# Kernel tuning notes

Measured on AMD Instinct MI355X. Metric: run time of the kernel, lower is better.

## Reference

```python
import jax, jax.numpy as jnp
import numpy as np

N, E, D, C, L, G = 50000, 1600000, 128, 10, 4, 512
BN_EPS = 1e-5


def setup_inputs() -> dict:
    key = jax.random.key(0)
    ks = jax.random.split(key, 16)
    s = 0.05  # weight init scale
    inp = {
        "x": jax.random.normal(ks[0], (N, D), dtype=jnp.float32),
        "edge_index": jax.random.randint(ks[1], (2, E), 0, N, dtype=jnp.int32),
        "batch": jnp.sort(jax.random.randint(ks[2], (N,), 0, G, dtype=jnp.int32)),
        "num_graphs": G,
        # GINConv inner MLP params (layer 0 input dim == D since num_features == num_hidden)
        "conv_W1": jax.random.normal(ks[3], (L, D, D), dtype=jnp.float32) * s,
        "conv_b1": jnp.zeros((L, D), dtype=jnp.float32),
        "conv_bn_g": jnp.ones((L, D), dtype=jnp.float32),
        "conv_bn_b": jnp.zeros((L, D), dtype=jnp.float32),
        "conv_W2": jax.random.normal(ks[4], (L, D, D), dtype=jnp.float32) * s,
        "conv_b2": jnp.zeros((L, D), dtype=jnp.float32),
        # outer BatchNorm after each conv
        "bn_g": jnp.ones((L, D), dtype=jnp.float32),
        "bn_b": jnp.zeros((L, D), dtype=jnp.float32),
        # per-scale classifier heads (L+1 of them; fcs[0] input dim == num_features == D)
        "fc_W": jax.random.normal(ks[5], (L + 1, D, C), dtype=jnp.float32) * s,
        "fc_b": jnp.zeros((L + 1, C), dtype=jnp.float32),
    }
    return inp


def _bn(h, g, b):
    # BatchNorm1d in training mode: batch stats over nodes, biased variance
    m = h.mean(axis=0)
    v = jnp.mean((h - m) ** 2, axis=0)
    return (h - m) * jax.lax.rsqrt(v + BN_EPS) * g + b


def reference(x, edge_index, batch, num_graphs, conv_W1, conv_b1, conv_bn_g,
              conv_bn_b, conv_W2, conv_b2, bn_g, bn_b, fc_W, fc_b):
    n_nodes = x.shape[0]
    src, dst = edge_index[0], edge_index[1]
    outs = [x]
    h = x
    for i in range(L):
        # GINConv (eps=0, aggr='add'): mlp(x + scatter_add of neighbor features)
        agg = jax.ops.segment_sum(h[src], dst, num_segments=n_nodes)  # [N, D]
        z = h + agg
        z = z @ conv_W1[i] + conv_b1[i]
        z = jax.nn.relu(_bn(z, conv_bn_g[i], conv_bn_b[i]))
        z = z @ conv_W2[i] + conv_b2[i]
        h = jax.nn.relu(_bn(z, bn_g[i], bn_b[i]))
        outs.append(h)
    out = None
    for i, o in enumerate(outs):
        pooled = jax.ops.segment_sum(o, batch, num_segments=num_graphs)  # [G, D]
        logits = pooled @ fc_W[i] + fc_b[i]
        out = logits if out is None else out + logits
    return jax.nn.log_softmax(out, axis=-1)
```

## Files before the change

kernel.cpp:

```cpp
#include <hip/hip_runtime.h>

#define NN 50000
#define EE 1600000
#define DD 128
#define CC 10
#define LLAY 4
#define GG 512
#define GD (GG*DD)
#define NB 196
#define BK_EDGES 6400
#define NSUB 16
#define SUBW 3125
#define WPAD 136

static constexpr float BN_EPS = 1e-5f;
static constexpr float INV_N = 1.0f / (float)NN;

typedef __bf16 bf16x8 __attribute__((ext_vector_type(8)));
typedef float f32x4 __attribute__((ext_vector_type(4)));

static __device__ __forceinline__ float bflo(unsigned u){ return __uint_as_float(u << 16); }
static __device__ __forceinline__ float bfhi(unsigned u){ return __uint_as_float(u & 0xffff0000u); }
static __device__ __forceinline__ unsigned short f2bf(float f){
    unsigned u = __float_as_uint(f);
    return (unsigned short)((u + 0x7fffu + ((u >> 16) & 1u)) >> 16);
}
static __device__ __forceinline__ unsigned packbf(float a, float b){
    return (unsigned)f2bf(a) | ((unsigned)f2bf(b) << 16);
}
static __device__ __forceinline__ bf16x8 ldfrag(const unsigned short* p){
    union { uint4 u; bf16x8 b; } t; t.u = *(const uint4*)p; return t.b;
}
static __device__ __forceinline__ bf16x8 asfrag(uint4 u){
    union { uint4 u; bf16x8 b; } t; t.u = u; return t.b;
}


__global__ void zero_k(int* p, int n){
    int i = blockIdx.x * 256 + threadIdx.x;
    if (i < n) p[i] = 0;
}

__global__ void wprep_k(const float* __restrict__ W1, const float* __restrict__ W2,
                        unsigned short* __restrict__ Wtall){
    int idx = blockIdx.x * 256 + threadIdx.x;
    int mat = idx >> 14; int rr = idx & 16383;
    int k = rr >> 7; int j = rr & 127;
    const float* Wsrc = (mat < 4) ? (W1 + mat * 16384) : (W2 + (mat - 4) * 16384);
    Wtall[mat * 16384 + j * 128 + k] = f2bf(Wsrc[k * 128 + j]);
}

__global__ __launch_bounds__(256) void bhist_k(const int* __restrict__ dstA,
                                               int* __restrict__ bucketCnt){
    __shared__ int c[NB];
    int tid = threadIdx.x;
    if (tid < NB) c[tid] = 0;
    __syncthreads();
    int e0 = blockIdx.x * BK_EDGES;
    for (int i = tid; i < BK_EDGES; i += 256){
        int e = e0 + i;
        if (e < EE) atomicAdd(&c[dstA[e] >> 8], 1);
    }
    __syncthreads();
    if (tid < NB && c[tid] > 0) atomicAdd(&bucketCnt[tid], c[tid]);
}

__global__ __launch_bounds__(256) void bscan_k(const int* __restrict__ bucketCnt,
                                               int* __restrict__ bucketBase,
                                               int* __restrict__ bucketCur,
                                               int* __restrict__ rp){
    __shared__ int lds[256];
    int t = threadIdx.x;
    int v = (t < NB) ? bucketCnt[t] : 0;
    lds[t] = v; __syncthreads();
    for (int o = 1; o < 256; o <<= 1){
        int xv = 0; if (t >= o) xv = lds[t - o];
        __syncthreads(); lds[t] += xv; __syncthreads();
    }
    int excl = lds[t] - v;
    if (t < NB){ bucketBase[t] = excl; bucketCur[t] = excl; }
    if (t == 0){ bucketBase[NB] = EE; rp[NN] = EE; }
}

__global__ void gsearch_k(const int* __restrict__ batch, int* __restrict__ gstart){
    int g = blockIdx.x * 256 + threadIdx.x;
    if (g <= GG){
        int lo = 0, hi = NN;
        while (lo < hi){ int mid = (lo + hi) >> 1; if (batch[mid] < g) lo = mid + 1; else hi = mid; }
        gstart[g] = lo;
    }
}

__global__ __launch_bounds__(256) void binA_k(const int* __restrict__ srcA,
                                              const int* __restrict__ dstA,
                                              int* __restrict__ bucketCur,
                                              unsigned* __restrict__ binned){
    __shared__ int cnt[NB], bas[NB], off[NB];
    int tid = threadIdx.x;
    if (tid < NB){ cnt[tid] = 0; off[tid] = 0; }
    __syncthreads();
    int e0 = blockIdx.x * BK_EDGES;
    for (int i = tid; i < BK_EDGES; i += 256){
        int e = e0 + i;
        if (e < EE) atomicAdd(&cnt[dstA[e] >> 8], 1);
    }
    __syncthreads();
    if (tid < NB && cnt[tid] > 0) bas[tid] = atomicAdd(&bucketCur[tid], cnt[tid]);
    __syncthreads();
    for (int i = tid; i < BK_EDGES; i += 256){
        int e = e0 + i;
        if (e < EE){
            int d = dstA[e]; int b = d >> 8;
            int p = bas[b] + atomicAdd(&off[b], 1);
            binned[p] = (unsigned)srcA[e] | ((unsigned)(d & 255) << 17);
        }
    }
}

__global__ __launch_bounds__(256) void binB_k(const unsigned* __restrict__ binned,
                                              const int* __restrict__ bucketBase,
                                              int* __restrict__ rp,
                                              int* __restrict__ ssort){
    __shared__ int c16[256 * NSUB];
    __shared__ int b16[256 * NSUB];
    __shared__ int nt[256];
    int b = blockIdx.x, tid = threadIdx.x;
    int nb0 = b * 256;
    int nmax = NN - nb0; if (nmax > 256) nmax = 256;
    #pragma unroll
    for (int k = 0; k < NSUB; k++) c16[tid * NSUB + k] = 0;
    __syncthreads();
    int base = bucketBase[b];
    int end  = bucketBase[b + 1];
    for (int i = base + tid; i < end; i += 256){
        unsigned u = binned[i];
        int src = (int)(u & 0x1FFFFu); int dl = (int)(u >> 17);
        atomicAdd(&c16[dl * NSUB + src / SUBW], 1);
    }
    __syncthreads();
    int cc[NSUB]; int tot = 0;
    #pragma unroll
    for (int k = 0; k < NSUB; k++){ cc[k] = c16[tid * NSUB + k]; tot += cc[k]; }
    nt[tid] = tot; __syncthreads();
    for (int o = 1; o < 256; o <<= 1){
        int xv = 0; if (tid >= o) xv = nt[tid - o];
        __syncthreads(); nt[tid] += xv; __syncthreads();
    }
    int p = base + nt[tid] - tot;
    if (tid < nmax) rp[nb0 + tid] = p;
    int run = p;
    #pragma unroll
    for (int k = 0; k < NSUB; k++){ b16[tid * NSUB + k] = run; run += cc[k]; }
    #pragma unroll
    for (int k = 0; k < NSUB; k++) c16[tid * NSUB + k] = 0;
    __syncthreads();
    for (int i = base + tid; i < end; i += 256){
        unsigned u = binned[i];
        int src = (int)(u & 0x1FFFFu); int dl = (int)(u >> 17);
        int t = src / SUBW;
        int pos = b16[dl * NSUB + t] + atomicAdd(&c16[dl * NSUB + t], 1);
        ssort[pos] = src;
    }
}

__global__ __launch_bounds__(256) void convxpool_k(const float2* __restrict__ x2,
                                                   const int* __restrict__ gstart,
                                                   unsigned* __restrict__ h32,
                                                   float* __restrict__ outp){
    __shared__ float sd[512];
    int b = blockIdx.x; int gid = b >> 2, chunk = b & 3;
    int tid = threadIdx.x; int c = tid & 63, rs = tid >> 6;
    int s = gstart[gid], e = gstart[gid + 1];
    float a0 = 0.f, a1 = 0.f;
    for (int n = s + chunk * 4 + rs; n < e; n += 16){
        float2 v = x2[n * 64 + c];
        h32[n * 64 + c] = packbf(v.x, v.y);
        a0 += v.x; a1 += v.y;
    }
    sd[tid] = a0; sd[256 + tid] = a1; __syncthreads();
    if (tid < 64){
        float r0 = 0.f, r1 = 0.f;
        #pragma unroll
        for (int k2 = 0; k2 < 4; k2++){ r0 += sd[tid + 64 * k2]; r1 += sd[256 + tid + 64 * k2]; }
        atomicAdd(&outp[gid * 128 + 2 * tid], r0);
        atomicAdd(&outp[gid * 128 + 2 * tid + 1], r1);
    }
}


__global__ __launch_bounds__(256) void agg_k(const unsigned* __restrict__ h32,
                                             const int* __restrict__ rp,
                                             const int* __restrict__ ssort,
                                             unsigned* __restrict__ z32,
                                             float* __restrict__ zstats){
    int tid = threadIdx.x;
    if (blockIdx.x == 0) zstats[tid] = 0.f;
    int n = blockIdx.x * 4 + (tid >> 6);
    int lane = tid & 63;
    unsigned self = h32[n * 64 + lane];
    float ax = bflo(self), ay = bfhi(self);
    int e  = __builtin_amdgcn_readfirstlane(rp[n]);
    int e1 = __builtin_amdgcn_readfirstlane(rp[n + 1]);
    for (; e + 15 < e1; e += 16){
        int sA[16];
        #pragma unroll
        for (int k = 0; k < 16; k++) sA[k] = ssort[e + k];
        unsigned uA[16];
        #pragma unroll
        for (int k = 0; k < 16; k++) uA[k] = h32[sA[k] * 64 + lane];
        #pragma unroll
        for (int k = 0; k < 16; k++){ ax += bflo(uA[k]); ay += bfhi(uA[k]); }
    }
    for (; e + 3 < e1; e += 4){
        int s0 = ssort[e], s1 = ssort[e + 1], s2 = ssort[e + 2], s3 = ssort[e + 3];
        unsigned u0 = h32[s0 * 64 + lane];
        unsigned u1 = h32[s1 * 64 + lane];
        unsigned u2 = h32[s2 * 64 + lane];
        unsigned u3 = h32[s3 * 64 + lane];
        ax += bflo(u0) + bflo(u1); ay += bfhi(u0) + bfhi(u1);
        ax += bflo(u2) + bflo(u3); ay += bfhi(u2) + bfhi(u3);
    }
    for (; e < e1; ++e){
        unsigned u0 = h32[ssort[e] * 64 + lane];
        ax += bflo(u0); ay += bfhi(u0);
    }
    z32[n * 64 + lane] = packbf(ax, ay);
}

template<int TR>
__global__ __launch_bounds__(256) void gemm_k(const unsigned* __restrict__ A32,
                                              const unsigned short* __restrict__ Wtg,
                                              const float* __restrict__ bias,
                                              unsigned short* __restrict__ Cst,
                                              const float* __restrict__ stats,
                                              const float* __restrict__ gma,
                                              const float* __restrict__ bta,
                                              float* __restrict__ ostats,
                                              float* __restrict__ zstats,
                                              float* __restrict__ zpool){
    __shared__ __align__(16) unsigned short Wl[64 * WPAD];
    __shared__ float sred[512];
    __shared__ __align__(16) float sl[128], tl[128];
    int tid = threadIdx.x;
    int slice = blockIdx.x & 1;
    int tileb = blockIdx.x >> 1;
    if (blockIdx.x == 0 && zstats) zstats[tid] = 0.f;
    if (zpool && blockIdx.x < 256) zpool[blockIdx.x * 256 + tid] = 0.f;
    {
        const uint4* src = (const uint4*)(Wtg + slice * 64 * 128);
        uint4* dst = (uint4*)Wl;
        #pragma unroll
        for (int i = 0; i < 4; i++){
            int idx = tid + 256 * i;
            int row = idx >> 4, c16 = idx & 15;
            dst[row * (WPAD / 8) + c16] = src[idx];
        }
    }
    if (TR && tid < 128){
        float mean = stats[tid] * INV_N;
        float q    = stats[128 + tid] * INV_N;
        float inv  = rsqrtf(q - mean * mean + BN_EPS);
        float s    = gma[tid] * inv;
        sl[tid] = s; tl[tid] = bta[tid] - mean * s;
    }
    __syncthreads();

    int wv = tid >> 6, lane = tid & 63;
    int rowbase = tileb * 128 + wv * 32;
    int r0 = rowbase + (lane & 15);
    int r1 = r0 + 16;
    int kd = (lane >> 4) * 4;

    uint4 va[4], vb[4];
    #pragma unroll
    for (int ks = 0; ks < 4; ks++){
        va[ks] = (r0 < NN) ? *(const uint4*)(A32 + r0 * 64 + ks * 16 + kd) : make_uint4(0,0,0,0);
        vb[ks] = (r1 < NN) ? *(const uint4*)(A32 + r1 * 64 + ks * 16 + kd) : make_uint4(0,0,0,0);
    }
    if (TR){
        #pragma unroll
        for (int ks = 0; ks < 4; ks++){
            int q = ks * 8 + (lane >> 4) * 2;
            float4 sA = ((const float4*)sl)[q], sB = ((const float4*)sl)[q + 1];
            float4 tA = ((const float4*)tl)[q], tB = ((const float4*)tl)[q + 1];
            float fs[8] = {sA.x, sA.y, sA.z, sA.w, sB.x, sB.y, sB.z, sB.w};
            float ft[8] = {tA.x, tA.y, tA.z, tA.w, tB.x, tB.y, tB.z, tB.w};
            unsigned* pa = (unsigned*)&va[ks];
            unsigned* pb = (unsigned*)&vb[ks];
            #pragma unroll
            for (int c = 0; c < 4; c++){
                float f0 = fmaxf(bflo(pa[c]) * fs[2*c] + ft[2*c], 0.f);
                float f1 = fmaxf(bfhi(pa[c]) * fs[2*c+1] + ft[2*c+1], 0.f);
                pa[c] = packbf(f0, f1);
                f0 = fmaxf(bflo(pb[c]) * fs[2*c] + ft[2*c], 0.f);
                f1 = fmaxf(bfhi(pb[c]) * fs[2*c+1] + ft[2*c+1], 0.f);
                pb[c] = packbf(f0, f1);
            }
        }
    }

    f32x4 acc[2][4];
    #pragma unroll
    for (int a = 0; a < 2; a++)
        #pragma unroll
        for (int b = 0; b < 4; b++) acc[a][b] = (f32x4){0.f, 0.f, 0.f, 0.f};

    #pragma unroll
    for (int ks = 0; ks < 4; ks++){
        int wk = ks * 32 + (lane >> 4) * 8;
        bf16x8 a0 = asfrag(va[ks]);
        bf16x8 a1 = asfrag(vb[ks]);
        #pragma unroll
        for (int ct = 0; ct < 4; ++ct){
            bf16x8 b = ldfrag(&Wl[(ct * 16 + (lane & 15)) * WPAD + wk]);
            acc[0][ct] = __builtin_amdgcn_mfma_f32_16x16x32_bf16(a0, b, acc[0][ct], 0, 0, 0);
            acc[1][ct] = __builtin_amdgcn_mfma_f32_16x16x32_bf16(a1, b, acc[1][ct], 0, 0, 0);
        }
    }

    int cl = lane & 15, rq = lane >> 4;
    float colS[4], colQ[4];
    #pragma unroll
    for (int ct = 0; ct < 4; ++ct){
        int col = slice * 64 + ct * 16 + cl;
        float bv = bias[col];
        float ps = 0.f, pq = 0.f;
        #pragma unroll
        for (int rt = 0; rt < 2; ++rt){
            #pragma unroll
            for (int rr2 = 0; rr2 < 4; ++rr2){
                int grow = rowbase + rt * 16 + rq * 4 + rr2;
                if (grow < NN){
                    float val = acc[rt][ct][rr2] + bv;
                    Cst[grow * 128 + col] = f2bf(val);
                    ps += val; pq += val * val;
                }
            }
        }
        ps += __shfl_xor(ps, 16); pq += __shfl_xor(pq, 16);
        ps += __shfl_xor(ps, 32); pq += __shfl_xor(pq, 32);
        colS[ct] = ps; colQ[ct] = pq;
    }
    if (rq == 0){
        #pragma unroll
        for (int ct = 0; ct < 4; ++ct){
            sred[wv * 64 + ct * 16 + cl]       = colS[ct];
            sred[256 + wv * 64 + ct * 16 + cl] = colQ[ct];
        }
    }
    __syncthreads();
    if (tid < 64){
        float s1 = sred[tid] + sred[64 + tid] + sred[128 + tid] + sred[192 + tid];
        float s2 = sred[256 + tid] + sred[320 + tid] + sred[384 + tid] + sred[448 + tid];
        atomicAdd(&ostats[slice * 64 + tid], s1);
        atomicAdd(&ostats[128 + slice * 64 + tid], s2);
    }
}

__global__ __launch_bounds__(256) void ewpool_k(const unsigned* __restrict__ z32,
                                                const float* __restrict__ stats,
                                                const float* __restrict__ g,
                                                const float* __restrict__ b,
                                                const int* __restrict__ gstart,
                                                unsigned* __restrict__ h32,
                                                float* __restrict__ outp){
    __shared__ float sd[512];
    int blk = blockIdx.x; int gid = blk >> 2, chunk = blk & 3;
    int tid = threadIdx.x;
    int c = tid & 63, rs = tid >> 6;
    int c2 = c * 2;
    float m0 = stats[c2] * INV_N,     q0 = stats[128 + c2] * INV_N;
    float inv0 = rsqrtf(q0 - m0 * m0 + BN_EPS);
    float s0 = g[c2] * inv0, t0 = b[c2] - m0 * s0;
    float m1 = stats[c2 + 1] * INV_N, q1 = stats[129 + c2] * INV_N;
    float inv1 = rsqrtf(q1 - m1 * m1 + BN_EPS);
    float s1 = g[c2 + 1] * inv1, t1 = b[c2 + 1] - m1 * s1;
    int s = gstart[gid], e = gstart[gid + 1];
    float a0 = 0.f, a1 = 0.f;
    int n = s + chunk * 4 + rs;
    for (; n + 16 < e; n += 32){
        unsigned u0 = z32[n * 64 + c];
        unsigned u1 = z32[(n + 16) * 64 + c];
        float f0, f1;
        f0 = fmaxf(bflo(u0) * s0 + t0, 0.f); f1 = fmaxf(bfhi(u0) * s1 + t1, 0.f);
        h32[n * 64 + c] = packbf(f0, f1); a0 += f0; a1 += f1;
        f0 = fmaxf(bflo(u1) * s0 + t0, 0.f); f1 = fmaxf(bfhi(u1) * s1 + t1, 0.f);
        h32[(n + 16) * 64 + c] = packbf(f0, f1); a0 += f0; a1 += f1;
    }
    for (; n < e; n += 16){
        unsigned u = z32[n * 64 + c];
        float f0 = fmaxf(bflo(u) * s0 + t0, 0.f);
        float f1 = fmaxf(bfhi(u) * s1 + t1, 0.f);
        h32[n * 64 + c] = packbf(f0, f1);
        a0 += f0; a1 += f1;
    }
    sd[tid] = a0; sd[256 + tid] = a1; __syncthreads();
    if (tid < 64){
        float r0 = 0.f, r1 = 0.f;
        #pragma unroll
        for (int k2 = 0; k2 < 4; k2++){ r0 += sd[tid + 64 * k2]; r1 += sd[256 + tid + 64 * k2]; }
        atomicAdd(&outp[gid * 128 + 2 * tid], r0);
        atomicAdd(&outp[gid * 128 + 2 * tid + 1], r1);
    }
}

__global__ __launch_bounds__(64) void final_k(const float* __restrict__ pooled,
                                              const float* __restrict__ fcW,
                                              const float* __restrict__ fcb,
                                              float* __restrict__ out){
    int g = blockIdx.x, l = threadIdx.x;
    float p0[5], p1[5];
    #pragma unroll
    for (int i = 0; i < 5; i++){
        p0[i] = pooled[i * GD + g * 128 + l];
        p1[i] = pooled[i * GD + g * 128 + 64 + l];
    }
    float lg[10];
    #pragma unroll
    for (int c2 = 0; c2 < 10; c2++){
        float s = 0;
        #pragma unroll
        for (int i = 0; i < 5; i++){
            s += p0[i] * fcW[(i * 128 + l) * 10 + c2];
            s += p1[i] * fcW[(i * 128 + 64 + l) * 10 + c2];
        }
        #pragma unroll
        for (int off = 32; off >= 1; off >>= 1) s += __shfl_down(s, off);
        lg[c2] = s;
    }
    if (l == 0){
        #pragma unroll
        for (int c2 = 0; c2 < 10; c2++){
            float bs = 0;
            #pragma unroll
            for (int i = 0; i < 5; i++) bs += fcb[i * 10 + c2];
            lg[c2] += bs;
        }
        float mx = lg[0];
        #pragma unroll
        for (int c2 = 1; c2 < 10; c2++) mx = fmaxf(mx, lg[c2]);
        float se = 0;
        #pragma unroll
        for (int c2 = 0; c2 < 10; c2++) se += expf(lg[c2] - mx);
        float lse = mx + logf(se);
        #pragma unroll
        for (int c2 = 0; c2 < 10; c2++) out[g * 10 + c2] = lg[c2] - lse;
    }
}


extern "C" void kernel_launch(void* const* d_in, const int* in_sizes, int n_in,
                              void* d_out, int out_size, void* d_ws, size_t ws_size,
                              hipStream_t stream){
    (void)in_sizes; (void)n_in; (void)out_size; (void)ws_size;
    const float* x     = (const float*)d_in[0];
    const int*   ei    = (const int*)d_in[1];
    const int*   batch = (const int*)d_in[2];
    const float* cW1   = (const float*)d_in[4];
    const float* cb1   = (const float*)d_in[5];
    const float* cbng  = (const float*)d_in[6];
    const float* cbnb  = (const float*)d_in[7];
    const float* cW2   = (const float*)d_in[8];
    const float* cb2   = (const float*)d_in[9];
    const float* bng   = (const float*)d_in[10];
    const float* bnb   = (const float*)d_in[11];
    const float* fcW   = (const float*)d_in[12];
    const float* fcb   = (const float*)d_in[13];

    char* base = (char*)d_ws;
    size_t off = 0;
    auto alloc = [&](size_t bytes) -> void* {
        void* p = base + off;
        off = (off + bytes + 255) & ~(size_t)255;
        return p;
    };
    unsigned*       hB     = (unsigned*)alloc((size_t)NN * 64 * 4);
    unsigned*       zA     = (unsigned*)alloc((size_t)NN * 64 * 4);
    unsigned*       zB     = (unsigned*)alloc((size_t)NN * 64 * 4);
    unsigned short* Wtall  = (unsigned short*)alloc(8 * 16384 * 2);
    int*            ssort  = (int*)alloc((size_t)EE * 4);
    int*            rp     = (int*)alloc((NN + 1) * 4);
    int*            gstart = (int*)alloc((GG + 1) * 4);
    int*            bucketCnt  = (int*)alloc(NB * 4);
    int*            bucketBase = (int*)alloc((NB + 1) * 4);
    int*            bucketCur  = (int*)alloc(NB * 4);
    float*          pooled = (float*)alloc((size_t)5 * GD * 4);
    float*          stats1 = (float*)alloc(256 * 4);
    float*          stats2 = (float*)alloc(256 * 4);
    unsigned*       binned = (unsigned*)zB;

    int zwords = (int)(((char*)(pooled + GD) - (char*)bucketCnt) / 4);

    zero_k<<<(zwords + 255) / 256, 256, 0, stream>>>(bucketCnt, zwords);
    wprep_k<<<512, 256, 0, stream>>>(cW1, cW2, Wtall);
    bhist_k<<<(EE + BK_EDGES - 1) / BK_EDGES, 256, 0, stream>>>(ei + EE, bucketCnt);
    bscan_k<<<1, 256, 0, stream>>>(bucketCnt, bucketBase, bucketCur, rp);
    gsearch_k<<<3, 256, 0, stream>>>(batch, gstart);
    binA_k<<<(EE + BK_EDGES - 1) / BK_EDGES, 256, 0, stream>>>(ei, ei + EE, bucketCur, binned);
    binB_k<<<NB, 256, 0, stream>>>(binned, bucketBase, rp, ssort);
    convxpool_k<<<4 * GG, 256, 0, stream>>>((const float2*)x, gstart, hB, pooled);

    const int gemmGrid = 2 * ((NN + 127) / 128);
    for (int i = 0; i < LLAY; i++){
        agg_k<<<NN / 4, 256, 0, stream>>>(hB, rp, ssort, zA, stats1);
        gemm_k<0><<<gemmGrid, 256, 0, stream>>>(zA, Wtall + i * 16384, cb1 + i * 128,
                                                (unsigned short*)zB,
                                                nullptr, nullptr, nullptr, stats1, stats2, nullptr);
        gemm_k<1><<<gemmGrid, 256, 0, stream>>>(zB, Wtall + (4 + i) * 16384, cb2 + i * 128,
                                                (unsigned short*)zA,
                                                stats1, cbng + i * 128, cbnb + i * 128, stats2, nullptr,
                                                pooled + (size_t)(i + 1) * GD);
        ewpool_k<<<4 * GG, 256, 0, stream>>>(zA, stats2, bng + i * 128, bnb + i * 128,
                                             gstart, hB, pooled + (size_t)(i + 1) * GD);
    }
    final_k<<<GG, 64, 0, stream>>>(pooled, fcW, fcb, (float*)d_out);
}
```

Baseline: 562.0 us.

## Bin edges into fixed-capacity buckets, widen sort blocks, halve GEMM row tiles

Edge binning now writes each destination bucket into a fixed-capacity slot, which removes the separate histogram pass, and runs the prefix scan after binning. The second sort pass now uses 1024-thread blocks. The GEMM tile drops from 128 to 64 rows per block, with one 16-row MFMA tile per wave, doubling the grid for better occupancy and CU coverage. The fixed bucket capacity assumes no bucket exceeds 16000 edges, which holds only for roughly uniform destinations, and the smaller tiles reuse each LDS weight load across fewer rows.

```diff
diff --git a/kernel.cpp b/kernel.cpp
--- a/kernel.cpp
+++ b/kernel.cpp
@@ -8,7 +8,8 @@
 #define GG 512
 #define GD (GG*DD)
 #define NB 196
-#define BK_EDGES 6400
+#define BK_EDGES 1600
+#define BUCKCAP 16000
 #define NSUB 16
 #define SUBW 3125
 #define WPAD 136
@@ -50,38 +51,6 @@
     Wtall[mat * 16384 + j * 128 + k] = f2bf(Wsrc[k * 128 + j]);
 }
 
-__global__ __launch_bounds__(256) void bhist_k(const int* __restrict__ dstA,
-                                               int* __restrict__ bucketCnt){
-    __shared__ int c[NB];
-    int tid = threadIdx.x;
-    if (tid < NB) c[tid] = 0;
-    __syncthreads();
-    int e0 = blockIdx.x * BK_EDGES;
-    for (int i = tid; i < BK_EDGES; i += 256){
-        int e = e0 + i;
-        if (e < EE) atomicAdd(&c[dstA[e] >> 8], 1);
-    }
-    __syncthreads();
-    if (tid < NB && c[tid] > 0) atomicAdd(&bucketCnt[tid], c[tid]);
-}
-
-__global__ __launch_bounds__(256) void bscan_k(const int* __restrict__ bucketCnt,
-                                               int* __restrict__ bucketBase,
-                                               int* __restrict__ bucketCur,
-                                               int* __restrict__ rp){
-    __shared__ int lds[256];
-    int t = threadIdx.x;
-    int v = (t < NB) ? bucketCnt[t] : 0;
-    lds[t] = v; __syncthreads();
-    for (int o = 1; o < 256; o <<= 1){
-        int xv = 0; if (t >= o) xv = lds[t - o];
-        __syncthreads(); lds[t] += xv; __syncthreads();
-    }
-    int excl = lds[t] - v;
-    if (t < NB){ bucketBase[t] = excl; bucketCur[t] = excl; }
-    if (t == 0){ bucketBase[NB] = EE; rp[NN] = EE; }
-}
-
 __global__ void gsearch_k(const int* __restrict__ batch, int* __restrict__ gstart){
     int g = blockIdx.x * 256 + threadIdx.x;
     if (g <= GG){
@@ -111,51 +80,76 @@
         int e = e0 + i;
         if (e < EE){
             int d = dstA[e]; int b = d >> 8;
-            int p = bas[b] + atomicAdd(&off[b], 1);
+            int p = b * BUCKCAP + bas[b] + atomicAdd(&off[b], 1);
             binned[p] = (unsigned)srcA[e] | ((unsigned)(d & 255) << 17);
         }
     }
 }
 
-__global__ __launch_bounds__(256) void binB_k(const unsigned* __restrict__ binned,
-                                              const int* __restrict__ bucketBase,
-                                              int* __restrict__ rp,
-                                              int* __restrict__ ssort){
+__global__ __launch_bounds__(256) void bscan_k(const int* __restrict__ bucketCur,
+                                               int* __restrict__ bucketBase,
+                                               int* __restrict__ rp){
+    __shared__ int lds[256];
+    int t = threadIdx.x;
+    int v = (t < NB) ? bucketCur[t] : 0;
+    lds[t] = v; __syncthreads();
+    for (int o = 1; o < 256; o <<= 1){
+        int xv = 0; if (t >= o) xv = lds[t - o];
+        __syncthreads(); lds[t] += xv; __syncthreads();
+    }
+    int excl = lds[t] - v;
+    if (t < NB) bucketBase[t] = excl;
+    if (t == 0){ bucketBase[NB] = EE; rp[NN] = EE; }
+}
+
+__global__ __launch_bounds__(1024) void binB_k(const unsigned* __restrict__ binned,
+                                               const int* __restrict__ bucketCur,
+                                               const int* __restrict__ bucketBase,
+                                               int* __restrict__ rp,
+                                               int* __restrict__ ssort){
     __shared__ int c16[256 * NSUB];
     __shared__ int b16[256 * NSUB];
     __shared__ int nt[256];
     int b = blockIdx.x, tid = threadIdx.x;
     int nb0 = b * 256;
     int nmax = NN - nb0; if (nmax > 256) nmax = 256;
-    #pragma unroll
-    for (int k = 0; k < NSUB; k++) c16[tid * NSUB + k] = 0;
-    __syncthreads();
+    for (int i = tid; i < 256 * NSUB; i += 1024) c16[i] = 0;
+    __syncthreads();
+    int cntb = bucketCur[b];
+    int src0 = b * BUCKCAP;
     int base = bucketBase[b];
-    int end  = bucketBase[b + 1];
-    for (int i = base + tid; i < end; i += 256){
-        unsigned u = binned[i];
+    for (int i = tid; i < cntb; i += 1024){
+        unsigned u = binned[src0 + i];
         int src = (int)(u & 0x1FFFFu); int dl = (int)(u >> 17);
         atomicAdd(&c16[dl * NSUB + src / SUBW], 1);
     }
     __syncthreads();
     int cc[NSUB]; int tot = 0;
-    #pragma unroll
-    for (int k = 0; k < NSUB; k++){ cc[k] = c16[tid * NSUB + k]; tot += cc[k]; }
-    nt[tid] = tot; __syncthreads();
+    if (tid < 256){
+        #pragma unroll
+        for (int k = 0; k < NSUB; k++){ cc[k] = c16[tid * NSUB + k]; tot += cc[k]; }
+        nt[tid] = tot;
+    }
+    __syncthreads();
     for (int o = 1; o < 256; o <<= 1){
-        int xv = 0; if (tid >= o) xv = nt[tid - o];
-        __syncthreads(); nt[tid] += xv; __syncthreads();
-    }
-    int p = base + nt[tid] - tot;
-    if (tid < nmax) rp[nb0 + tid] = p;
-    int run = p;
-    #pragma unroll
-    for (int k = 0; k < NSUB; k++){ b16[tid * NSUB + k] = run; run += cc[k]; }
-    #pragma unroll
-    for (int k = 0; k < NSUB; k++) c16[tid * NSUB + k] = 0;
-    __syncthreads();
-    for (int i = base + tid; i < end; i += 256){
-        unsigned u = binned[i];
+        int xv = 0;
+        if (tid < 256 && tid >= o) xv = nt[tid - o];
+        __syncthreads();
+        if (tid < 256) nt[tid] += xv;
+        __syncthreads();
+    }
+    if (tid < 256){
+        int p = base + nt[tid] - tot;
+        if (tid < nmax) rp[nb0 + tid] = p;
+        int run = p;
+        #pragma unroll
+        for (int k = 0; k < NSUB; k++){ b16[tid * NSUB + k] = run; run += cc[k]; }
+    }
+    __syncthreads();
+    for (int i = tid; i < 256 * NSUB; i += 1024) c16[i] = 0;
+    __syncthreads();
+    for (int i = tid; i < cntb; i += 1024){
+        unsigned u = binned[src0 + i];
         int src = (int)(u & 0x1FFFFu); int dl = (int)(u >> 17);
         int t = src / SUBW;
         int pos = b16[dl * NSUB + t] + atomicAdd(&c16[dl * NSUB + t], 1);
@@ -266,17 +260,14 @@
     __syncthreads();
 
     int wv = tid >> 6, lane = tid & 63;
-    int rowbase = tileb * 128 + wv * 32;
+    int rowbase = tileb * 64 + wv * 16;
     int r0 = rowbase + (lane & 15);
-    int r1 = r0 + 16;
     int kd = (lane >> 4) * 4;
 
-    uint4 va[4], vb[4];
-    #pragma unroll
-    for (int ks = 0; ks < 4; ks++){
+    uint4 va[4];
+    #pragma unroll
+    for (int ks = 0; ks < 4; ks++)
         va[ks] = (r0 < NN) ? *(const uint4*)(A32 + r0 * 64 + ks * 16 + kd) : make_uint4(0,0,0,0);
-        vb[ks] = (r1 < NN) ? *(const uint4*)(A32 + r1 * 64 + ks * 16 + kd) : make_uint4(0,0,0,0);
-    }
     if (TR){
         #pragma unroll
         for (int ks = 0; ks < 4; ks++){
@@ -286,35 +277,27 @@
             float fs[8] = {sA.x, sA.y, sA.z, sA.w, sB.x, sB.y, sB.z, sB.w};
             float ft[8] = {tA.x, tA.y, tA.z, tA.w, tB.x, tB.y, tB.z, tB.w};
             unsigned* pa = (unsigned*)&va[ks];
-            unsigned* pb = (unsigned*)&vb[ks];
             #pragma unroll
             for (int c = 0; c < 4; c++){
                 float f0 = fmaxf(bflo(pa[c]) * fs[2*c] + ft[2*c], 0.f);
                 float f1 = fmaxf(bfhi(pa[c]) * fs[2*c+1] + ft[2*c+1], 0.f);
                 pa[c] = packbf(f0, f1);
-                f0 = fmaxf(bflo(pb[c]) * fs[2*c] + ft[2*c], 0.f);
-                f1 = fmaxf(bfhi(pb[c]) * fs[2*c+1] + ft[2*c+1], 0.f);
-                pb[c] = packbf(f0, f1);
             }
         }
     }
 
-    f32x4 acc[2][4];
-    #pragma unroll
-    for (int a = 0; a < 2; a++)
-        #pragma unroll
-        for (int b = 0; b < 4; b++) acc[a][b] = (f32x4){0.f, 0.f, 0.f, 0.f};
+    f32x4 acc[4];
+    #pragma unroll
+    for (int b = 0; b < 4; b++) acc[b] = (f32x4){0.f, 0.f, 0.f, 0.f};
 
     #pragma unroll
     for (int ks = 0; ks < 4; ks++){
         int wk = ks * 32 + (lane >> 4) * 8;
         bf16x8 a0 = asfrag(va[ks]);
-        bf16x8 a1 = asfrag(vb[ks]);
         #pragma unroll
         for (int ct = 0; ct < 4; ++ct){
             bf16x8 b = ldfrag(&Wl[(ct * 16 + (lane & 15)) * WPAD + wk]);
-            acc[0][ct] = __builtin_amdgcn_mfma_f32_16x16x32_bf16(a0, b, acc[0][ct], 0, 0, 0);
-            acc[1][ct] = __builtin_amdgcn_mfma_f32_16x16x32_bf16(a1, b, acc[1][ct], 0, 0, 0);
+            acc[ct] = __builtin_amdgcn_mfma_f32_16x16x32_bf16(a0, b, acc[ct], 0, 0, 0);
         }
     }
 
@@ -326,15 +309,12 @@
         float bv = bias[col];
         float ps = 0.f, pq = 0.f;
         #pragma unroll
-        for (int rt = 0; rt < 2; ++rt){
-            #pragma unroll
-            for (int rr2 = 0; rr2 < 4; ++rr2){
-                int grow = rowbase + rt * 16 + rq * 4 + rr2;
-                if (grow < NN){
-                    float val = acc[rt][ct][rr2] + bv;
-                    Cst[grow * 128 + col] = f2bf(val);
-                    ps += val; pq += val * val;
-                }
+        for (int rr2 = 0; rr2 < 4; ++rr2){
+            int grow = rowbase + rq * 4 + rr2;
+            if (grow < NN){
+                float val = acc[ct][rr2] + bv;
+                Cst[grow * 128 + col] = f2bf(val);
+                ps += val; pq += val * val;
             }
         }
         ps += __shfl_xor(ps, 16); pq += __shfl_xor(pq, 16);
@@ -481,7 +461,6 @@
     int*            ssort  = (int*)alloc((size_t)EE * 4);
     int*            rp     = (int*)alloc((NN + 1) * 4);
     int*            gstart = (int*)alloc((GG + 1) * 4);
-    int*            bucketCnt  = (int*)alloc(NB * 4);
     int*            bucketBase = (int*)alloc((NB + 1) * 4);
     int*            bucketCur  = (int*)alloc(NB * 4);
     float*          pooled = (float*)alloc((size_t)5 * GD * 4);
@@ -489,18 +468,17 @@
     float*          stats2 = (float*)alloc(256 * 4);
     unsigned*       binned = (unsigned*)zB;
 
-    int zwords = (int)(((char*)(pooled + GD) - (char*)bucketCnt) / 4);
-
-    zero_k<<<(zwords + 255) / 256, 256, 0, stream>>>(bucketCnt, zwords);
+    int zwords = (int)(((char*)(pooled + GD) - (char*)bucketCur) / 4);
+
+    zero_k<<<(zwords + 255) / 256, 256, 0, stream>>>(bucketCur, zwords);
     wprep_k<<<512, 256, 0, stream>>>(cW1, cW2, Wtall);
-    bhist_k<<<(EE + BK_EDGES - 1) / BK_EDGES, 256, 0, stream>>>(ei + EE, bucketCnt);
-    bscan_k<<<1, 256, 0, stream>>>(bucketCnt, bucketBase, bucketCur, rp);
     gsearch_k<<<3, 256, 0, stream>>>(batch, gstart);
     binA_k<<<(EE + BK_EDGES - 1) / BK_EDGES, 256, 0, stream>>>(ei, ei + EE, bucketCur, binned);
-    binB_k<<<NB, 256, 0, stream>>>(binned, bucketBase, rp, ssort);
+    bscan_k<<<1, 256, 0, stream>>>(bucketCur, bucketBase, rp);
+    binB_k<<<NB, 1024, 0, stream>>>(binned, bucketCur, bucketBase, rp, ssort);
     convxpool_k<<<4 * GG, 256, 0, stream>>>((const float2*)x, gstart, hB, pooled);
 
-    const int gemmGrid = 2 * ((NN + 127) / 128);
+    const int gemmGrid = 2 * ((NN + 63) / 64);
     for (int i = 0; i < LLAY; i++){
         agg_k<<<NN / 4, 256, 0, stream>>>(hB, rp, ssort, zA, stats1);
         gemm_k<0><<<gemmGrid, 256, 0, stream>>>(zA, Wtall + i * 16384, cb1 + i * 128,
```

Measured after the change: 605.2 us. +7.7%, slower.
